# Optimization experiments

Hardware: AMD Instinct MI355X
Metric: run time of the kernel (lower is better)

The kernel has to match this reference:

```python
import jax, jax.numpy as jnp
import numpy as np

OUT = 7            # output_size
SR = 2             # sampling_ratio
SCALES = (0.25, 0.125, 0.0625, 0.03125)  # P2..P5
CANON_S = 224.0
CANON_L = 4.0
LVL_EPS = 1e-6
K_MIN, K_MAX = 2, 5  # -log2(scales[0]), -log2(scales[-1])


def setup_inputs() -> dict:
    key = jax.random.key(0)
    ks = jax.random.split(key, 6)
    B, C, N = 2, 256, 256
    sizes = (200, 100, 50, 25)
    inp = {}
    for i, (k, hw) in enumerate(zip(ks[:4], sizes)):
        inp[f"feat{i}"] = jax.random.normal(k, (B, C, hw, hw), dtype=jnp.float32)
    x1y1 = jax.random.uniform(ks[4], (B, N, 2), minval=0.0, maxval=600.0)
    wh = jax.random.uniform(ks[5], (B, N, 2), minval=16.0, maxval=256.0)
    boxes = jnp.concatenate([x1y1, jnp.minimum(x1y1 + wh, 800.0)], axis=-1)
    inp["boxes"] = boxes.astype(jnp.float32)
    return inp


def _roi_align(feat, rois, scale):
    """torchvision RoIAlign (aligned=False). feat [B,C,H,W], rois [N,5] (bidx,x1,y1,x2,y2)."""
    B, C, H, W = feat.shape
    bidx = rois[:, 0].astype(jnp.int32)
    x1 = rois[:, 1] * scale
    y1 = rois[:, 2] * scale
    x2 = rois[:, 3] * scale
    y2 = rois[:, 4] * scale
    roi_w = jnp.maximum(x2 - x1, 1.0)
    roi_h = jnp.maximum(y2 - y1, 1.0)
    bin_h = roi_h / OUT
    bin_w = roi_w / OUT
    g = jnp.arange(OUT * SR)
    bin_idx = (g // SR).astype(feat.dtype)
    sub = (g % SR).astype(feat.dtype) + 0.5
    # sample coordinates [N, G] with G = OUT*SR
    ys = y1[:, None] + bin_idx * bin_h[:, None] + sub * bin_h[:, None] / SR
    xs = x1[:, None] + bin_idx * bin_w[:, None] + sub * bin_w[:, None] / SR
    vy = (ys >= -1.0) & (ys <= H)
    vx = (xs >= -1.0) & (xs <= W)
    y = jnp.clip(ys, 0.0, H - 1.0)
    x = jnp.clip(xs, 0.0, W - 1.0)
    y0 = jnp.floor(y).astype(jnp.int32)
    x0 = jnp.floor(x).astype(jnp.int32)
    y1i = jnp.minimum(y0 + 1, H - 1)
    x1i = jnp.minimum(x0 + 1, W - 1)
    ly = y - y0
    lx = x - x0
    hy = 1.0 - ly
    hx = 1.0 - lx

    def gather(yi, xi):
        # advanced indices at dims 0,2,3 with slice at dim 1 -> [N, G, G, C]
        return feat[bidx[:, None, None], :, yi[:, :, None], xi[:, None, :]]

    v = (gather(y0, x0) * (hy[:, :, None] * hx[:, None, :])[..., None]
         + gather(y0, x1i) * (hy[:, :, None] * lx[:, None, :])[..., None]
         + gather(y1i, x0) * (ly[:, :, None] * hx[:, None, :])[..., None]
         + gather(y1i, x1i) * (ly[:, :, None] * lx[:, None, :])[..., None])
    mask = (vy[:, :, None] & vx[:, None, :])[..., None]
    v = jnp.where(mask, v, 0.0)                       # [N, G, G, C]
    n = v.shape[0]
    v = v.reshape(n, OUT, SR, OUT, SR, C).mean(axis=(2, 4))  # avg pool per bin
    return jnp.transpose(v, (0, 3, 1, 2))             # [N, C, OUT, OUT]


def reference(feat0, feat1, feat2, feat3, boxes):
    feats = [feat0, feat1, feat2, feat3]
    B, N = boxes.shape[:2]
    flat = boxes.reshape(B * N, 4)
    ids = jnp.repeat(jnp.arange(B, dtype=flat.dtype), N)[:, None]
    rois = jnp.concatenate([ids, flat], axis=1)       # [B*N, 5]
    # FPN level assignment heuristic (LevelMapper)
    area = (flat[:, 2] - flat[:, 0]) * (flat[:, 3] - flat[:, 1])
    s = jnp.sqrt(area)
    lvl = jnp.floor(CANON_L + jnp.log2(s / CANON_S) + LVL_EPS)
    levels = jnp.clip(lvl, K_MIN, K_MAX).astype(jnp.int32) - K_MIN
    # Pool every roi at every level (static shapes), then select by level,
    # equivalent math to the gather/scatter-merge in the original.
    pooled = jnp.stack([_roi_align(f, rois, sc) for f, sc in zip(feats, SCALES)], axis=0)
    return pooled[levels, jnp.arange(B * N)]          # [B*N, C, OUT, OUT]
```

## Files before the change

kernel.cpp:

```cpp
#include <hip/hip_runtime.h>
#include <hip/hip_fp16.h>


#define ROI_OUT 7
#define NSAMP   14
#define C_TOT   256
#define N_PER_B 256
#define BINS    49
#define TOT_HW  53125

#define NTILE_X 832

#define SWZG(c) ((((c) ^ ((c) >> 3)) & 7) << 2)

typedef const __attribute__((address_space(1))) float* gas1_t;
typedef __attribute__((address_space(3))) float*       las3_t;

__global__ __launch_bounds__(256)
void repack_kernel(const float* __restrict__ f0, const float* __restrict__ f1,
                   const float* __restrict__ f2, const float* __restrict__ f3,
                   __half* __restrict__ ws)
{
    __shared__ float tile[64 * 64];

    const int tx = blockIdx.x;
    const float* feat; int HW, base, hw0;
    if (tx < 625)      { feat = f0; HW = 40000; base = 0;     hw0 = tx * 64; }
    else if (tx < 782) { feat = f1; HW = 10000; base = 40000; hw0 = (tx - 625) * 64; }
    else if (tx < 822) { feat = f2; HW = 2500;  base = 50000; hw0 = (tx - 782) * 64; }
    else               { feat = f3; HW = 625;   base = 52500; hw0 = (tx - 822) * 64; }

    const int g  = blockIdx.y;
    const int c0 = g * 64;
    const int b  = blockIdx.z;
    const float* src = feat + ((size_t)(b * C_TOT + c0)) * (size_t)HW + hw0;

    const int t = threadIdx.x;
    const int w = t >> 6;
    const int l = t & 63;

    const bool fast = (hw0 + 64 <= HW) && ((HW & 3) == 0);

    if (fast) {
        const int cq = l >> 4;
        const int hl = (l & 15) * 4;
        #pragma unroll
        for (int i = 0; i < 4; ++i) {
            int q = 4 * w + i;
            int c = 4 * q + cq;
            const float* gp = src + (size_t)c * HW + (hl ^ SWZG(c));
            __builtin_amdgcn_global_load_lds((gas1_t)(const void*)gp,
                                             (las3_t)(void*)(tile + q * 256),
                                             16, 0, 0);
        }
    } else {
        const int hl = (t & 15) * 4;
        const int cr = t >> 4;
        #pragma unroll
        for (int i = 0; i < 4; ++i) {
            int c  = cr + 16 * i;
            int ps = hl ^ SWZG(c);
            #pragma unroll
            for (int j = 0; j < 4; ++j) {
                int srchw = ps + j;
                float v = (srchw < HW - hw0) ? src[(size_t)c * HW + srchw] : 0.0f;
                tile[c * 64 + hl + j] = v;
            }
        }
    }
    __syncthreads();

    __half* plane = ws + ((size_t)b * TOT_HW + base) * C_TOT
                       + (size_t)g * (size_t)HW * 64 + (size_t)hw0 * 64;
    const int c4 = (l & 15) * 4;
    #pragma unroll
    for (int i = 0; i < 4; ++i) {
        int hw = 16 * w + 4 * i + (l >> 4);
        if (hw0 + hw < HW) {
            float v0 = tile[(c4 + 0) * 64 + (hw ^ SWZG(c4 + 0))];
            float v1 = tile[(c4 + 1) * 64 + (hw ^ SWZG(c4 + 1))];
            float v2 = tile[(c4 + 2) * 64 + (hw ^ SWZG(c4 + 2))];
            float v3 = tile[(c4 + 3) * 64 + (hw ^ SWZG(c4 + 3))];
            __half2 hh[2];
            hh[0] = __floats2half2_rn(v0, v1);
            hh[1] = __floats2half2_rn(v2, v3);
            *(float2*)(plane + (size_t)hw * 64 + c4) = *(const float2*)hh;
        }
    }
}

__global__ __launch_bounds__(256)
void msroi_main(const __half* __restrict__ ws, const float* __restrict__ boxes,
                float* __restrict__ out)
{
    __shared__ float oacc[C_TOT * BINS];
    __shared__ int4  pY[NSAMP], pX[NSAMP];

    const int tid = threadIdx.x;
    const int roi = blockIdx.x;
    const int b   = roi >> 8;

    const float* bxp = boxes + (size_t)roi * 4;
    float bx1 = bxp[0], by1 = bxp[1], bx2 = bxp[2], by2 = bxp[3];
    float area = (bx2 - bx1) * (by2 - by1);
    float s    = sqrtf(area);
    float lvlf = floorf(4.0f + log2f(s * (1.0f / 224.0f)) + 1e-6f);
    lvlf = fminf(fmaxf(lvlf, 2.0f), 5.0f);
    int level = (int)lvlf - 2;

    int H, W, lvbase; float scale;
    switch (level) {
        case 0:  H = 200; W = 200; lvbase = 0;     scale = 0.25f;    break;
        case 1:  H = 100; W = 100; lvbase = 40000; scale = 0.125f;   break;
        case 2:  H = 50;  W = 50;  lvbase = 50000; scale = 0.0625f;  break;
        default: H = 25;  W = 25;  lvbase = 52500; scale = 0.03125f; break;
    }

    float x1 = bx1 * scale, y1 = by1 * scale;
    float roi_w = fmaxf(bx2 * scale - x1, 1.0f);
    float roi_h = fmaxf(by2 * scale - y1, 1.0f);
    float bin_w = roi_w * (1.0f / ROI_OUT);
    float bin_h = roi_h * (1.0f / ROI_OUT);

    if (tid < 2 * NSAMP) {
        bool isy = tid >= NSAMP;
        int  j   = isy ? tid - NSAMP : tid;
        int  pb  = j >> 1, sub = j & 1;
        float start = isy ? y1 : x1;
        float bsz   = isy ? bin_h : bin_w;
        int   lim   = isy ? H : W;
        float ss = start + (float)pb * bsz + ((float)sub + 0.5f) * bsz * 0.5f;
        float v  = (ss >= -1.0f && ss <= (float)lim) ? 1.0f : 0.0f;
        float cc = fminf(fmaxf(ss, 0.0f), (float)lim - 1.0f);
        int   i0 = (int)floorf(cc);
        int   i1 = min(i0 + 1, lim - 1);
        float l  = cc - (float)i0;
        int4 pk; pk.x = i0; pk.y = i1;
        pk.z = __float_as_int(l); pk.w = __float_as_int(v);
        if (isy) pY[j] = pk; else pX[j] = pk;
    }
    __syncthreads();

    const int wave = tid >> 6;
    const int lane = tid & 63;
    const int c    = lane * 4;
    const __half* gbase = ws + ((size_t)b * TOT_HW + lvbase) * C_TOT
                             + (size_t)(lane >> 4) * (size_t)(H * W) * 64
                             + (lane & 15) * 4;

    for (int bin = wave; bin < BINS; bin += 4) {
        int ph = bin / ROI_OUT;
        int pw = bin - ph * ROI_OUT;
        float a0 = 0.f, a1 = 0.f, a2 = 0.f, a3 = 0.f;

        #pragma unroll
        for (int sy = 0; sy < 2; ++sy) {
            int4 py  = pY[2 * ph + sy];
            float ly = __int_as_float(py.z);
            float vy = __int_as_float(py.w);
            float hy = 1.0f - ly;
            #pragma unroll
            for (int sx = 0; sx < 2; ++sx) {
                int4 px  = pX[2 * pw + sx];
                float lx = __int_as_float(px.z);
                float vv = vy * __int_as_float(px.w);
                float hx = 1.0f - lx;
                float w00 = vv * hy * hx, w01 = vv * hy * lx;
                float w10 = vv * ly * hx, w11 = vv * ly * lx;

                const __half2* p00 = (const __half2*)(gbase + (size_t)(py.x * W + px.x) * 64);
                const __half2* p01 = (const __half2*)(gbase + (size_t)(py.x * W + px.y) * 64);
                const __half2* p10 = (const __half2*)(gbase + (size_t)(py.y * W + px.x) * 64);
                const __half2* p11 = (const __half2*)(gbase + (size_t)(py.y * W + px.y) * 64);

                float2 g0, g1;
                g0 = __half22float2(p00[0]); g1 = __half22float2(p00[1]);
                a0 += w00 * g0.x; a1 += w00 * g0.y; a2 += w00 * g1.x; a3 += w00 * g1.y;
                g0 = __half22float2(p01[0]); g1 = __half22float2(p01[1]);
                a0 += w01 * g0.x; a1 += w01 * g0.y; a2 += w01 * g1.x; a3 += w01 * g1.y;
                g0 = __half22float2(p10[0]); g1 = __half22float2(p10[1]);
                a0 += w10 * g0.x; a1 += w10 * g0.y; a2 += w10 * g1.x; a3 += w10 * g1.y;
                g0 = __half22float2(p11[0]); g1 = __half22float2(p11[1]);
                a0 += w11 * g0.x; a1 += w11 * g0.y; a2 += w11 * g1.x; a3 += w11 * g1.y;
            }
        }
        oacc[(c + 0) * BINS + bin] = a0 * 0.25f;
        oacc[(c + 1) * BINS + bin] = a1 * 0.25f;
        oacc[(c + 2) * BINS + bin] = a2 * 0.25f;
        oacc[(c + 3) * BINS + bin] = a3 * 0.25f;
    }
    __syncthreads();

    float4*       o4 = (float4*)(out + (size_t)roi * (C_TOT * BINS));
    const float4* s4 = (const float4*)oacc;
    for (int j = tid; j < (C_TOT * BINS) / 4; j += 256) o4[j] = s4[j];
}

__global__ __launch_bounds__(256)
void msroi_direct(const float* __restrict__ f0, const float* __restrict__ f1,
                  const float* __restrict__ f2, const float* __restrict__ f3,
                  const float* __restrict__ boxes, float* __restrict__ out, int total)
{
    int e = blockIdx.x * 256 + threadIdx.x;
    if (e >= total) return;
    int bin = e % BINS;
    int c   = (e / BINS) % C_TOT;
    int roi = e / (BINS * C_TOT);
    int b   = roi / N_PER_B;

    const float* bx = boxes + (size_t)roi * 4;
    float bx1 = bx[0], by1 = bx[1], bx2 = bx[2], by2 = bx[3];
    float area = (bx2 - bx1) * (by2 - by1);
    float s    = sqrtf(area);
    float lvlf = floorf(4.0f + log2f(s * (1.0f / 224.0f)) + 1e-6f);
    lvlf = fminf(fmaxf(lvlf, 2.0f), 5.0f);
    int level = (int)lvlf - 2;

    const float* feat; int H, W; float scale;
    switch (level) {
        case 0:  feat = f0; H = 200; W = 200; scale = 0.25f;    break;
        case 1:  feat = f1; H = 100; W = 100; scale = 0.125f;   break;
        case 2:  feat = f2; H = 50;  W = 50;  scale = 0.0625f;  break;
        default: feat = f3; H = 25;  W = 25;  scale = 0.03125f; break;
    }
    float x1 = bx1 * scale, y1 = by1 * scale;
    float roi_w = fmaxf(bx2 * scale - x1, 1.0f);
    float roi_h = fmaxf(by2 * scale - y1, 1.0f);
    float bin_w = roi_w * (1.0f / ROI_OUT);
    float bin_h = roi_h * (1.0f / ROI_OUT);
    int ph = bin / ROI_OUT, pw = bin - ph * ROI_OUT;
    const float* plane = feat + ((size_t)(b * C_TOT + c)) * (size_t)(H * W);
    float Hf = (float)H, Wf = (float)W, acc = 0.0f;
    #pragma unroll
    for (int sy = 0; sy < 2; ++sy) {
        float ys = y1 + (float)ph * bin_h + ((float)sy + 0.5f) * bin_h * 0.5f;
        float vy = (ys >= -1.0f && ys <= Hf) ? 1.0f : 0.0f;
        float y  = fminf(fmaxf(ys, 0.0f), Hf - 1.0f);
        int   y0 = (int)floorf(y);
        int   y1i = min(y0 + 1, H - 1);
        float ly = y - (float)y0, hy = 1.0f - ly;
        int ro0 = y0 * W, ro1 = y1i * W;
        #pragma unroll
        for (int sx = 0; sx < 2; ++sx) {
            float xs = x1 + (float)pw * bin_w + ((float)sx + 0.5f) * bin_w * 0.5f;
            float vx = (xs >= -1.0f && xs <= Wf) ? 1.0f : 0.0f;
            float x  = fminf(fmaxf(xs, 0.0f), Wf - 1.0f);
            int   x0 = (int)floorf(x);
            int   x1i = min(x0 + 1, W - 1);
            float lx = x - (float)x0, hx = 1.0f - lx;
            float v00 = plane[ro0 + x0],  v01 = plane[ro0 + x1i];
            float v10 = plane[ro1 + x0],  v11 = plane[ro1 + x1i];
            acc += vy * vx * (hy * (hx * v00 + lx * v01) + ly * (hx * v10 + lx * v11));
        }
    }
    out[e] = acc * 0.25f;
}

extern "C" void kernel_launch(void* const* d_in, const int* in_sizes, int n_in,
                              void* d_out, int out_size, void* d_ws, size_t ws_size,
                              hipStream_t stream)
{
    const float* f0    = (const float*)d_in[0];
    const float* f1    = (const float*)d_in[1];
    const float* f2    = (const float*)d_in[2];
    const float* f3    = (const float*)d_in[3];
    const float* boxes = (const float*)d_in[4];
    float* out = (float*)d_out;

    const size_t ws_needed = (size_t)2 * TOT_HW * C_TOT * sizeof(__half);
    if (ws_size >= ws_needed) {
        __half* ws = (__half*)d_ws;
        hipLaunchKernelGGL(repack_kernel, dim3(NTILE_X, 4, 2), dim3(256), 0, stream,
                           f0, f1, f2, f3, ws);
        hipLaunchKernelGGL(msroi_main, dim3(2 * N_PER_B), dim3(256), 0, stream,
                           ws, boxes, out);
    } else {
        int total = out_size;
        hipLaunchKernelGGL(msroi_direct, dim3((total + 255) / 256), dim3(256), 0, stream,
                           f0, f1, f2, f3, boxes, out, total);
    }
}
```

Baseline: 50.95 us.

## Make repack kernel persistent with double-buffered async LDS loads over tile chunks

The repack kernel now has each block process a chunk of seven 64-wide tiles. The global-to-LDS load of the next tile is issued before the current one is converted and stored, with explicit vmcnt waits and barriers managing the two buffers. Partial and tail tiles (the f1/f2 tail tiles and all of f3) go to a separate set of scalar blocks. The goal is to hide load latency and cut block launch overhead. The cost is fewer blocks in flight and more LDS per block, which can reduce parallelism, and the hand-written vmcnt counts are fragile.

```diff
diff --git a/kernel.cpp b/kernel.cpp
--- a/kernel.cpp
+++ b/kernel.cpp
@@ -9,83 +9,150 @@
 #define BINS    49
 #define TOT_HW  53125
 
-#define NTILE_X 832
+#define FAST_PER_GB   820
+#define CHUNK         7
+#define FBLK_PER_GB   118
+#define NFASTBLK      (FBLK_PER_GB * 8)
+#define NSCALBLK      (12 * 8)
+#define NBLK          (NFASTBLK + NSCALBLK)
 
 #define SWZG(c) ((((c) ^ ((c) >> 3)) & 7) << 2)
 
 typedef const __attribute__((address_space(1))) float* gas1_t;
 typedef __attribute__((address_space(3))) float*       las3_t;
 
-__global__ __launch_bounds__(256)
-void repack_kernel(const float* __restrict__ f0, const float* __restrict__ f1,
-                   const float* __restrict__ f2, const float* __restrict__ f3,
-                   __half* __restrict__ ws)
-{
-    __shared__ float tile[64 * 64];
-
-    const int tx = blockIdx.x;
-    const float* feat; int HW, base, hw0;
-    if (tx < 625)      { feat = f0; HW = 40000; base = 0;     hw0 = tx * 64; }
-    else if (tx < 782) { feat = f1; HW = 10000; base = 40000; hw0 = (tx - 625) * 64; }
-    else if (tx < 822) { feat = f2; HW = 2500;  base = 50000; hw0 = (tx - 782) * 64; }
-    else               { feat = f3; HW = 625;   base = 52500; hw0 = (tx - 822) * 64; }
-
-    const int g  = blockIdx.y;
-    const int c0 = g * 64;
-    const int b  = blockIdx.z;
-    const float* src = feat + ((size_t)(b * C_TOT + c0)) * (size_t)HW + hw0;
-
-    const int t = threadIdx.x;
-    const int w = t >> 6;
-    const int l = t & 63;
-
-    const bool fast = (hw0 + 64 <= HW) && ((HW & 3) == 0);
-
-    if (fast) {
-        const int cq = l >> 4;
-        const int hl = (l & 15) * 4;
-        #pragma unroll
-        for (int i = 0; i < 4; ++i) {
-            int q = 4 * w + i;
-            int c = 4 * q + cq;
-            const float* gp = src + (size_t)c * HW + (hl ^ SWZG(c));
-            __builtin_amdgcn_global_load_lds((gas1_t)(const void*)gp,
-                                             (las3_t)(void*)(tile + q * 256),
-                                             16, 0, 0);
-        }
-    } else {
-        const int hl = (t & 15) * 4;
-        const int cr = t >> 4;
-        #pragma unroll
-        for (int i = 0; i < 4; ++i) {
-            int c  = cr + 16 * i;
-            int ps = hl ^ SWZG(c);
-            #pragma unroll
-            for (int j = 0; j < 4; ++j) {
-                int srchw = ps + j;
-                float v = (srchw < HW - hw0) ? src[(size_t)c * HW + srchw] : 0.0f;
-                tile[c * 64 + hl + j] = v;
-            }
-        }
-    }
-    __syncthreads();
-
-    __half* plane = ws + ((size_t)b * TOT_HW + base) * C_TOT
-                       + (size_t)g * (size_t)HW * 64 + (size_t)hw0 * 64;
+#define WAITV(n) asm volatile("s_waitcnt vmcnt(" #n ")" ::: "memory")
+#define BAR()    asm volatile("s_barrier" ::: "memory")
+
+struct UnitGeom { const float* feat; int HW; int base; int hw0; };
+
+__device__ __forceinline__ UnitGeom fast_geom(int f, const float* f0,
+                                              const float* f1, const float* f2)
+{
+    UnitGeom u;
+    if (f < 625)      { u.feat = f0; u.HW = 40000; u.base = 0;     u.hw0 = f * 64; }
+    else if (f < 781) { u.feat = f1; u.HW = 10000; u.base = 40000; u.hw0 = (f - 625) * 64; }
+    else              { u.feat = f2; u.HW = 2500;  u.base = 50000; u.hw0 = (f - 781) * 64; }
+    return u;
+}
+
+__device__ __forceinline__ void unit_issue(const float* src, int HW, int w, int l,
+                                           float* buf)
+{
+    const int cq = l >> 4;
+    const int hl = (l & 15) * 4;
+    #pragma unroll
+    for (int i = 0; i < 4; ++i) {
+        int q = 4 * w + i;
+        int c = 4 * q + cq;
+        const float* gp = src + (size_t)c * HW + (hl ^ SWZG(c));
+        __builtin_amdgcn_global_load_lds((gas1_t)(const void*)gp,
+                                         (las3_t)(void*)(buf + q * 256),
+                                         16, 0, 0);
+    }
+}
+
+__device__ __forceinline__ void unit_store(const float* buf, __half* plane,
+                                           int hw0, int HW, int w, int l)
+{
     const int c4 = (l & 15) * 4;
     #pragma unroll
     for (int i = 0; i < 4; ++i) {
         int hw = 16 * w + 4 * i + (l >> 4);
         if (hw0 + hw < HW) {
-            float v0 = tile[(c4 + 0) * 64 + (hw ^ SWZG(c4 + 0))];
-            float v1 = tile[(c4 + 1) * 64 + (hw ^ SWZG(c4 + 1))];
-            float v2 = tile[(c4 + 2) * 64 + (hw ^ SWZG(c4 + 2))];
-            float v3 = tile[(c4 + 3) * 64 + (hw ^ SWZG(c4 + 3))];
+            float v0 = buf[(c4 + 0) * 64 + (hw ^ SWZG(c4 + 0))];
+            float v1 = buf[(c4 + 1) * 64 + (hw ^ SWZG(c4 + 1))];
+            float v2 = buf[(c4 + 2) * 64 + (hw ^ SWZG(c4 + 2))];
+            float v3 = buf[(c4 + 3) * 64 + (hw ^ SWZG(c4 + 3))];
             __half2 hh[2];
             hh[0] = __floats2half2_rn(v0, v1);
             hh[1] = __floats2half2_rn(v2, v3);
             *(float2*)(plane + (size_t)hw * 64 + c4) = *(const float2*)hh;
         }
+    }
+}
+
+__global__ __launch_bounds__(256)
+void repack_kernel(const float* __restrict__ f0, const float* __restrict__ f1,
+                   const float* __restrict__ f2, const float* __restrict__ f3,
+                   __half* __restrict__ ws)
+{
+    __shared__ float tileA[64 * 64];
+    __shared__ float tileB[64 * 64];
+
+    const int t = threadIdx.x;
+    const int w = t >> 6;
+    const int l = t & 63;
+    const int p = blockIdx.x;
+
+    if (p < NFASTBLK) {
+        const int gb = p / FBLK_PER_GB;
+        const int k  = p - gb * FBLK_PER_GB;
+        const int g  = gb >> 1;
+        const int b  = gb & 1;
+        const int fbeg = k * CHUNK;
+        const int fend = min(fbeg + CHUNK, FAST_PER_GB);
+        const int n    = fend - fbeg;
+        if (n <= 0) return;
+
+        const int c0 = g * 64;
+
+        UnitGeom u0 = fast_geom(fbeg, f0, f1, f2);
+        unit_issue(u0.feat + ((size_t)(b * C_TOT + c0)) * (size_t)u0.HW + u0.hw0,
+                   u0.HW, w, l, tileA);
+
+        for (int i = 0; i < n; ++i) {
+            float* cur = (i & 1) ? tileB : tileA;
+            float* nxt = (i & 1) ? tileA : tileB;
+            const bool hn = (i + 1 < n);
+
+            if (hn) {
+                UnitGeom un = fast_geom(fbeg + i + 1, f0, f1, f2);
+                unit_issue(un.feat + ((size_t)(b * C_TOT + c0)) * (size_t)un.HW + un.hw0,
+                           un.HW, w, l, nxt);
+            }
+            if (i == 0) { if (hn) WAITV(4); else WAITV(0); }
+            else        { if (hn) WAITV(8); else WAITV(4); }
+            BAR();
+
+            UnitGeom uc = fast_geom(fbeg + i, f0, f1, f2);
+            __half* plane = ws + ((size_t)b * TOT_HW + uc.base) * C_TOT
+                               + (size_t)g * (size_t)uc.HW * 64
+                               + (size_t)uc.hw0 * 64;
+            unit_store(cur, plane, uc.hw0, uc.HW, w, l);
+            BAR();
+        }
+    } else {
+        const int su = p - NFASTBLK;
+        const int gb = su / 12;
+        const int s  = su - gb * 12;
+        const int g  = gb >> 1;
+        const int b  = gb & 1;
+        const int c0 = g * 64;
+
+        const float* feat; int HW, base, hw0;
+        if (s == 0)      { feat = f1; HW = 10000; base = 40000; hw0 = 9984; }
+        else if (s == 1) { feat = f2; HW = 2500;  base = 50000; hw0 = 2496; }
+        else             { feat = f3; HW = 625;   base = 52500; hw0 = (s - 2) * 64; }
+
+        const float* src = feat + ((size_t)(b * C_TOT + c0)) * (size_t)HW + hw0;
+
+        for (int G = t; G < 64 * 16; G += 256) {
+            int c  = G >> 4;
+            int q  = G & 15;
+            int sh = (q * 4) ^ SWZG(c);
+            #pragma unroll
+            for (int j = 0; j < 4; ++j) {
+                int srchw = sh + j;
+                float v = (srchw < HW - hw0) ? src[(size_t)c * HW + srchw] : 0.0f;
+                tileA[c * 64 + q * 4 + j] = v;
+            }
+        }
+        __syncthreads();
+
+        __half* plane = ws + ((size_t)b * TOT_HW + base) * C_TOT
+                           + (size_t)g * (size_t)HW * 64 + (size_t)hw0 * 64;
+        unit_store(tileA, plane, hw0, HW, w, l);
     }
 }
 
@@ -270,7 +337,7 @@
     const size_t ws_needed = (size_t)2 * TOT_HW * C_TOT * sizeof(__half);
     if (ws_size >= ws_needed) {
         __half* ws = (__half*)d_ws;
-        hipLaunchKernelGGL(repack_kernel, dim3(NTILE_X, 4, 2), dim3(256), 0, stream,
+        hipLaunchKernelGGL(repack_kernel, dim3(NBLK), dim3(256), 0, stream,
                            f0, f1, f2, f3, ws);
         hipLaunchKernelGGL(msroi_main, dim3(2 * N_PER_B), dim3(256), 0, stream,
                            ws, boxes, out);
```

Result: faster. 49.62 us (-2.6%).
